# Kernel optimization log

Measured on AMD Instinct MI355X. Metric: run time of the kernel, lower is better.

## Reference

```python
import jax, jax.numpy as jnp
import numpy as np

N, C_IN, H, W = 32, 256, 56, 56
C_OUT, KH, KW = 256, 3, 3
ACT_BITS = 8


def setup_inputs() -> dict:
    key = jax.random.key(0)
    k_x, k_w, k_s, k_b = jax.random.split(key, 4)
    x = jax.random.normal(k_x, (N, C_IN, H, W), dtype=jnp.float32)
    # ternary weights in {-1, 0, +1}, stored as int8
    w_q = jax.random.randint(k_w, (C_OUT, C_IN, KH, KW), -1, 2).astype(jnp.int8)
    # per-output-channel scale, broadcastable over NCHW as [C,1,1]
    s = (jax.random.uniform(k_s, (C_OUT, 1, 1), dtype=jnp.float32) * 0.02 + 0.005)
    bias = jax.random.normal(k_b, (C_OUT,), dtype=jnp.float32) * 0.1
    act_s = jnp.float32(1.0 / 127.0)  # per-tensor activation quant scale
    return {"x": x, "w_q": w_q, "s": s, "bias": bias, "act_s": act_s}


def reference(x, w_q, s, bias, act_s):
    # activation fake-quant: clamp to [-1,1], round to act_bits symmetric grid
    qmax = (1 << (ACT_BITS - 1)) - 1  # 127
    x = jnp.clip(x, -1.0, 1.0)
    x_int = jnp.clip(jnp.round(x / act_s), -qmax, qmax)
    xq = x_int * act_s
    # ternary conv (weights upcast to float), stride 1, pad 1, dilation 1
    y = jax.lax.conv_general_dilated(
        xq, w_q.astype(jnp.float32),
        window_strides=(1, 1), padding=((1, 1), (1, 1)),
        lhs_dilation=(1, 1), rhs_dilation=(1, 1),
        dimension_numbers=("NCHW", "OIHW", "NCHW"), feature_group_count=1)
    # per-output-channel scale + bias
    y = y * s + bias.reshape(1, -1, 1, 1)
    return y
```

## Files before the change

### kernel.cpp

```cpp
#include <hip/hip_runtime.h>

typedef int v4i __attribute__((ext_vector_type(4)));

#define NIMG 32
#define CIN  256
#define COUT 256
#define HW   3136
#define W56  56
#define HP   58
#define PIMG (HP * HP)
#define WP_BYTES  (9 * COUT * CIN)
#define XQP_BYTES (NIMG * PIMG * CIN)
#define RBYTES    (4 * HP * 256)

#define VMCNT0()  asm volatile("s_waitcnt vmcnt(0)" ::: "memory")

__device__ __forceinline__ void gll16(const void* g, void* l)
{
    __builtin_amdgcn_global_load_lds(
        (const __attribute__((address_space(1))) int*)g,
        (__attribute__((address_space(3))) int*)l, 16, 0, 0);
}

__global__ __launch_bounds__(256) void zero_border(v4i* __restrict__ p)
{
    int i = blockIdx.x * 256 + threadIdx.x;
    if (i >= NIMG * 228 * 16) return;
    int n = i / 3648, r = i % 3648, pix = r >> 4, c = r & 15;
    int h, w;
    if (pix < 58)       { h = 0;         w = pix;       }
    else if (pix < 116) { h = 57;        w = pix - 58;  }
    else if (pix < 172) { h = pix - 115; w = 0;         }
    else                { h = pix - 171; w = 57;        }
    v4i z = {0, 0, 0, 0};
    p[(size_t)(n * PIMG + h * HP + w) * 16 + c] = z;
}

__global__ __launch_bounds__(256) void quantize_pad(
    const float* __restrict__ x, signed char* __restrict__ xqp)
{
    __shared__ int tile[64][65];
    const int n  = blockIdx.z;
    const int c0 = blockIdx.y * 64;
    const int p0 = blockIdx.x * 64;
    const int tid = threadIdx.x;

    const int px   = tid & 63;
    const int crow = tid >> 6;
    const float* xb = x + ((size_t)(n * CIN + c0)) * HW + p0;
#pragma unroll
    for (int i = 0; i < 16; ++i) {
        int c = crow + i * 4;
        float v = xb[(size_t)c * HW + px];
        v = fminf(fmaxf(v, -1.f), 1.f);
        tile[c][px] = (int)rintf(v * 127.f);
    }
    __syncthreads();

    const int c4   = tid & 15;
    const int prow = tid >> 4;
#pragma unroll
    for (int i = 0; i < 4; ++i) {
        int p  = prow + i * 16;
        int hw = p0 + p;
        int oh = hw / W56, ow = hw % W56;
        int b0 = tile[c4 * 4 + 0][p] & 255;
        int b1 = tile[c4 * 4 + 1][p] & 255;
        int b2 = tile[c4 * 4 + 2][p] & 255;
        int b3 = tile[c4 * 4 + 3][p] & 255;
        int packed = b0 | (b1 << 8) | (b2 << 16) | (b3 << 24);
        *(int*)(xqp + ((size_t)(n * PIMG + (oh + 1) * HP + (ow + 1))) * CIN
                    + c0 + c4 * 4) = packed;
    }
}

__global__ __launch_bounds__(256) void repack_w(
    const int* __restrict__ wq, signed char* __restrict__ wp2)
{
    int idx  = blockIdx.x * 256 + threadIdx.x;
    int t    = idx >> 16;
    int rem  = idx & 65535;
    int kc   = rem >> 14;
    int rem2 = rem & 16383;
    int co   = rem2 >> 6;
    int c6   = rem2 & 63;
    int ci   = kc * 64 + c6;
    wp2[idx] = (signed char)wq[(co * CIN + ci) * 9 + t];
}

__global__ __launch_bounds__(256, 2) void bitconv_conv(
    const signed char* __restrict__ xqp, const signed char* __restrict__ wp2,
    const float* __restrict__ scale, const float* __restrict__ bias,
    const float* __restrict__ act_s_p, float* __restrict__ out)
{
    __shared__ signed char Bq[RBYTES];

    const int tid  = threadIdx.x;
    const int lane = tid & 63;
    const int wid  = tid >> 6;
    const int l15  = lane & 15;
    const int kg   = lane >> 4;

    const int b  = blockIdx.x;
    const int w  = (b & 7) * 112 + (b >> 3);
    const int n  = w / 28;
    const int r0 = (w % 28) * 2;

    {
        const signed char* rsrc = xqp + ((size_t)n * PIMG + r0 * HP) * 256;
        const int base = wid * 64;
#pragma unroll
        for (int it = 0; it < 14; ++it) {
            int g   = it * 256 + base + lane;
            int pix = g >> 4, ch = g & 15;
            int src = pix * 256 + ((ch ^ (pix & 7)) << 4);
            gll16(rsrc + src, Bq + (it * 256 + base) * 16);
        }
        if (wid < 2) {
            int g   = 3584 + base + lane;
            int pix = g >> 4, ch = g & 15;
            int src = pix * 256 + ((ch ^ (pix & 7)) << 4);
            gll16(rsrc + src, Bq + (3584 + base) * 16);
        }
        VMCNT0();
        __syncthreads();
    }

    int ppj[7];
#pragma unroll
    for (int j = 0; j < 7; ++j) {
        int opx  = j * 16 + l15;
        int orow = opx / 56, ocol = opx % 56;
        ppj[j] = (orow + 1) * HP + (ocol + 1);
    }

    const signed char* ap = wp2 + (wid * 64 + l15) * 64 + kg * 16;
    v4i aa[2][4];
#pragma unroll
    for (int i = 0; i < 4; ++i) aa[0][i] = *(const v4i*)(ap + i * 1024);

    v4i acc[4][7] = {};
    const signed char* aps = ap;

    for (int t9 = 0; t9 < 9; ++t9) {
        const int pshift = (t9 / 3 - 1) * HP + (t9 % 3 - 1);
        int q[7];
#pragma unroll
        for (int j = 0; j < 7; ++j) {
            int pix = ppj[j] + pshift;
            q[j] = pix * 256 ^ (kg << 4) ^ ((pix & 7) << 4);
        }
#pragma unroll
        for (int kc = 0; kc < 4; ++kc) {
            const int cu = kc & 1, nx = cu ^ 1;
            const signed char* an = aps + 16384;
#pragma unroll
            for (int i = 0; i < 4; ++i)
                aa[nx][i] = *(const v4i*)(an + i * 1024);

            __builtin_amdgcn_s_setprio(1);
#pragma unroll
            for (int j = 0; j < 7; ++j) {
                v4i bb = *(const v4i*)(Bq + (q[j] ^ (kc << 6)));
#pragma unroll
                for (int i = 0; i < 4; ++i)
                    acc[i][j] = __builtin_amdgcn_mfma_i32_16x16x64_i8(
                        aa[cu][i], bb, acc[i][j], 0, 0, 0);
            }
            __builtin_amdgcn_s_setprio(0);
            aps = an;
        }
    }

    const float a_s = act_s_p[0];
    const int hw0 = r0 * W56;
#pragma unroll
    for (int i = 0; i < 4; ++i) {
        int cb = wid * 64 + i * 16 + kg * 4;
        float sc[4], bi[4];
#pragma unroll
        for (int r = 0; r < 4; ++r) {
            sc[r] = a_s * scale[cb + r];
            bi[r] = bias[cb + r];
        }
#pragma unroll
        for (int j = 0; j < 7; ++j) {
            int px = j * 16 + l15;
#pragma unroll
            for (int r = 0; r < 4; ++r)
                out[((size_t)(n * COUT + cb + r)) * HW + hw0 + px] =
                    (float)acc[i][j][r] * sc[r] + bi[r];
        }
    }
}

extern "C" void kernel_launch(void* const* d_in, const int* in_sizes, int n_in,
                              void* d_out, int out_size, void* d_ws, size_t ws_size,
                              hipStream_t stream)
{
    const float* x     = (const float*)d_in[0];
    const int*   w_q   = (const int*)d_in[1];
    const float* s     = (const float*)d_in[2];
    const float* bias  = (const float*)d_in[3];
    const float* act_s = (const float*)d_in[4];

    signed char* wp2 = (signed char*)d_ws;
    signed char* xqp = (signed char*)d_ws + WP_BYTES;

    zero_border<<<(NIMG * 228 * 16 + 255) / 256, 256, 0, stream>>>((v4i*)xqp);
    quantize_pad<<<dim3(49, 4, NIMG), 256, 0, stream>>>(x, xqp);
    repack_w<<<dim3(WP_BYTES / 256), 256, 0, stream>>>(w_q, wp2);
    bitconv_conv<<<dim3(NIMG * 28), 256, 0, stream>>>(
        xqp, wp2, s, bias, act_s, (float*)d_out);
}
```

Before: 85.97 us.

## Split conv blocks by output-channel halves and stage input channels in two LDS passes

Each conv block now computes 128 output channels instead of 256, doubling the grid to 1792 blocks. The LDS input tile is halved by loading 128 input channels at a time in two passes. Accumulators per wave drop from 4x7 to 2x7, and launch bounds are raised to 4 blocks per CU. The aim is more resident waves and better latency hiding. The cost is that every input row tile is loaded twice from global memory (once per output-channel half), plus an extra barrier per block.

```diff
diff --git a/kernel.cpp b/kernel.cpp
--- a/kernel.cpp
+++ b/kernel.cpp
@@ -11,7 +11,8 @@
 #define PIMG (HP * HP)
 #define WP_BYTES  (9 * COUT * CIN)
 #define XQP_BYTES (NIMG * PIMG * CIN)
-#define RBYTES    (4 * HP * 256)
+#define RHBYTES   (4 * HP * 128)
+#define RHGRAN    (4 * HP * 8)
 
 #define VMCNT0()  asm volatile("s_waitcnt vmcnt(0)" ::: "memory")
 
@@ -88,12 +89,12 @@
     wp2[idx] = (signed char)wq[(co * CIN + ci) * 9 + t];
 }
 
-__global__ __launch_bounds__(256, 2) void bitconv_conv(
+__global__ __launch_bounds__(256, 4) void bitconv_conv(
     const signed char* __restrict__ xqp, const signed char* __restrict__ wp2,
     const float* __restrict__ scale, const float* __restrict__ bias,
     const float* __restrict__ act_s_p, float* __restrict__ out)
 {
-    __shared__ signed char Bq[RBYTES];
+    __shared__ signed char Bq[RHBYTES];
 
     const int tid  = threadIdx.x;
     const int lane = tid & 63;
@@ -101,30 +102,12 @@
     const int l15  = lane & 15;
     const int kg   = lane >> 4;
 
-    const int b  = blockIdx.x;
-    const int w  = (b & 7) * 112 + (b >> 3);
-    const int n  = w / 28;
-    const int r0 = (w % 28) * 2;
-
-    {
-        const signed char* rsrc = xqp + ((size_t)n * PIMG + r0 * HP) * 256;
-        const int base = wid * 64;
-#pragma unroll
-        for (int it = 0; it < 14; ++it) {
-            int g   = it * 256 + base + lane;
-            int pix = g >> 4, ch = g & 15;
-            int src = pix * 256 + ((ch ^ (pix & 7)) << 4);
-            gll16(rsrc + src, Bq + (it * 256 + base) * 16);
-        }
-        if (wid < 2) {
-            int g   = 3584 + base + lane;
-            int pix = g >> 4, ch = g & 15;
-            int src = pix * 256 + ((ch ^ (pix & 7)) << 4);
-            gll16(rsrc + src, Bq + (3584 + base) * 16);
-        }
-        VMCNT0();
-        __syncthreads();
-    }
+    const int b     = blockIdx.x;
+    const int w     = (b & 7) * 224 + (b >> 3);
+    const int cout0 = (w & 1) * 128;
+    const int w2    = w >> 1;
+    const int n     = w2 / 28;
+    const int r0    = (w2 % 28) * 2;
 
     int ppj[7];
 #pragma unroll
@@ -134,49 +117,66 @@
         ppj[j] = (orow + 1) * HP + (ocol + 1);
     }
 
-    const signed char* ap = wp2 + (wid * 64 + l15) * 64 + kg * 16;
-    v4i aa[2][4];
-#pragma unroll
-    for (int i = 0; i < 4; ++i) aa[0][i] = *(const v4i*)(ap + i * 1024);
-
-    v4i acc[4][7] = {};
-    const signed char* aps = ap;
-
-    for (int t9 = 0; t9 < 9; ++t9) {
-        const int pshift = (t9 / 3 - 1) * HP + (t9 % 3 - 1);
-        int q[7];
-#pragma unroll
-        for (int j = 0; j < 7; ++j) {
-            int pix = ppj[j] + pshift;
-            q[j] = pix * 256 ^ (kg << 4) ^ ((pix & 7) << 4);
-        }
-#pragma unroll
-        for (int kc = 0; kc < 4; ++kc) {
-            const int cu = kc & 1, nx = cu ^ 1;
-            const signed char* an = aps + 16384;
-#pragma unroll
-            for (int i = 0; i < 4; ++i)
-                aa[nx][i] = *(const v4i*)(an + i * 1024);
-
-            __builtin_amdgcn_s_setprio(1);
+    const signed char* ap = wp2 + (cout0 + wid * 32 + l15) * 64 + kg * 16;
+
+    v4i acc[2][7] = {};
+
+    for (int h = 0; h < 2; ++h) {
+        if (h) __syncthreads();
+
+        const signed char* rsrc =
+            xqp + ((size_t)n * PIMG + r0 * HP) * 256 + h * 128;
+#pragma unroll
+        for (int it = 0; it < 8; ++it) {
+            int g = it * 256 + tid;
+            if (g < RHGRAN) {
+                int pix = g >> 3, ch = g & 7;
+                gll16(rsrc + pix * 256 + ((ch ^ (pix & 7)) << 4),
+                      Bq + g * 16);
+            }
+        }
+        VMCNT0();
+        __syncthreads();
+
+        const signed char* aps = ap + (2 * h) * 16384;
+        v4i aa0 = *(const v4i*)(aps);
+        v4i aa1 = *(const v4i*)(aps + 1024);
+
+        for (int t9 = 0; t9 < 9; ++t9) {
+            const int pshift = (t9 / 3 - 1) * HP + (t9 % 3 - 1);
+            int q[7];
 #pragma unroll
             for (int j = 0; j < 7; ++j) {
-                v4i bb = *(const v4i*)(Bq + (q[j] ^ (kc << 6)));
-#pragma unroll
-                for (int i = 0; i < 4; ++i)
-                    acc[i][j] = __builtin_amdgcn_mfma_i32_16x16x64_i8(
-                        aa[cu][i], bb, acc[i][j], 0, 0, 0);
+                int pix = ppj[j] + pshift;
+                q[j] = pix * 128 ^ ((pix & 7) << 4) ^ (kg << 4);
             }
-            __builtin_amdgcn_s_setprio(0);
-            aps = an;
+#pragma unroll
+            for (int kcw = 0; kcw < 2; ++kcw) {
+                const signed char* an = aps + (kcw == 0 ? 16384 : 65536);
+                v4i n0 = *(const v4i*)(an);
+                v4i n1 = *(const v4i*)(an + 1024);
+
+                __builtin_amdgcn_s_setprio(1);
+#pragma unroll
+                for (int j = 0; j < 7; ++j) {
+                    v4i bb = *(const v4i*)(Bq + (q[j] ^ (kcw << 6)));
+                    acc[0][j] = __builtin_amdgcn_mfma_i32_16x16x64_i8(
+                        aa0, bb, acc[0][j], 0, 0, 0);
+                    acc[1][j] = __builtin_amdgcn_mfma_i32_16x16x64_i8(
+                        aa1, bb, acc[1][j], 0, 0, 0);
+                }
+                __builtin_amdgcn_s_setprio(0);
+                aa0 = n0; aa1 = n1;
+            }
+            aps += 65536;
         }
     }
 
     const float a_s = act_s_p[0];
     const int hw0 = r0 * W56;
 #pragma unroll
-    for (int i = 0; i < 4; ++i) {
-        int cb = wid * 64 + i * 16 + kg * 4;
+    for (int i = 0; i < 2; ++i) {
+        int cb = cout0 + wid * 32 + i * 16 + kg * 4;
         float sc[4], bi[4];
 #pragma unroll
         for (int r = 0; r < 4; ++r) {
@@ -210,6 +210,6 @@
     zero_border<<<(NIMG * 228 * 16 + 255) / 256, 256, 0, stream>>>((v4i*)xqp);
     quantize_pad<<<dim3(49, 4, NIMG), 256, 0, stream>>>(x, xqp);
     repack_w<<<dim3(WP_BYTES / 256), 256, 0, stream>>>(w_q, wp2);
-    bitconv_conv<<<dim3(NIMG * 28), 256, 0, stream>>>(
+    bitconv_conv<<<dim3(NIMG * 28 * 2), 256, 0, stream>>>(
         xqp, wp2, s, bias, act_s, (float*)d_out);
 }
```

After: 158.2 us. +84.1%, slower.
